# Optimization experiments

Hardware: AMD Instinct MI355X
Metric: run time of the kernel (lower is better)

The kernel has to match this reference:

```python
import jax, jax.numpy as jnp
import numpy as np

B, N, D = 4, 2048, 512

def setup_inputs() -> dict:
    key = jax.random.key(0)
    ks = jax.random.split(key, 7)
    s = 1.0 / np.sqrt(D)
    return {
        "x": jax.random.normal(ks[0], (B, N, D), dtype=jnp.float32),
        "Wq": jax.random.uniform(ks[1], (D, D), jnp.float32, -s, s),
        "bq": jax.random.uniform(ks[2], (D,), jnp.float32, -s, s),
        "Wk": jax.random.uniform(ks[3], (D, D), jnp.float32, -s, s),
        "bk": jax.random.uniform(ks[4], (D,), jnp.float32, -s, s),
        "Wv": jax.random.uniform(ks[5], (D, D), jnp.float32, -s, s),
        "bv": jax.random.uniform(ks[6], (D,), jnp.float32, -s, s),
    }

def reference(x, Wq, bq, Wk, bk, Wv, bv):
    # QKV projections (torch Linear: y = x @ W^T + b)
    q = jnp.einsum('bnd,ed->bne', x, Wq) + bq
    k = jnp.einsum('bnd,ed->bne', x, Wk) + bk
    v = jnp.einsum('bnd,ed->bne', x, Wv) + bv
    scale = 1.0 / jnp.sqrt(jnp.asarray(q.shape[-1], q.dtype))
    scores = jnp.einsum('bqd,bkd->bqk', q, k) * scale  # [B,N,N]
    weights = jax.nn.softmax(scores, axis=-1)
    return jnp.einsum('bqk,bkd->bqd', weights, v)
```

## Files before the change

kernel.cpp:

```cpp
#include <hip/hip_runtime.h>
#include <cstdint>
#include <cstddef>

#define SEQ 2048
#define DIM 512

using floatx4 = __attribute__((ext_vector_type(4))) float;
using halfx8  = __attribute__((ext_vector_type(8))) _Float16;

__device__ __forceinline__ ushort f2h(float f) {
    _Float16 h = (_Float16)f;
    return __builtin_bit_cast(unsigned short, h);
}

__global__ void prep_k(const float* __restrict__ x,
                       const float* __restrict__ Wq, const float* __restrict__ Wk,
                       const float* __restrict__ Wv,
                       const float* __restrict__ bq, const float* __restrict__ bk,
                       const float* __restrict__ bv,
                       ushort* __restrict__ xh, ushort* __restrict__ wcat,
                       float* __restrict__ bcat, float* __restrict__ rowsum) {
    int i = blockIdx.x * 256 + threadIdx.x;
    if (i < 1048576) {
        float4 v = ((const float4*)x)[i];
        ((ushort4*)xh)[i] = make_ushort4(f2h(v.x), f2h(v.y), f2h(v.z), f2h(v.w));
    } else if (i < 1048576 + 196608) {
        int j = i - 1048576;
        int which = j >> 16;
        const float* w = (which == 0) ? Wq : (which == 1) ? Wk : Wv;
        float4 v = ((const float4*)w)[j & 0xFFFF];
        ((ushort4*)wcat)[j] = make_ushort4(f2h(v.x), f2h(v.y), f2h(v.z), f2h(v.w));
    } else if (i < 1048576 + 196608 + 384) {
        int j = i - 1245184;
        const float* bsrc = (j < 128) ? bq : (j < 256) ? bk : bv;
        ((float4*)bcat)[j] = ((const float4*)bsrc)[j & 127];
    } else if (i < 1048576 + 196608 + 384 + 2048) {
        int j = i - 1245568;
        ((float4*)rowsum)[j] = (float4){0.f, 0.f, 0.f, 0.f};
    }
}


template<int EPI>
__global__ __launch_bounds__(512, 4)
void gemm_k(const ushort* __restrict__ A, const ushort* __restrict__ B,
            void* __restrict__ Cout, const float* __restrict__ bias,
            float* __restrict__ rowsum, ushort* __restrict__ vt,
            int lda, int ldb, int ldc, int kIters, float alpha,
            long sA, long sB, long sC)
{
    __shared__ __align__(16) ushort As[2][8192];
    __shared__ __align__(16) ushort Bs[2][4096];
    ushort* Ps = &As[0][0];

    const int tid = threadIdx.x;
    const int bz = blockIdx.z;
    int b, kofs;
    if (EPI == 2) { b = bz & 3; kofs = (bz >> 2) * 512; }
    else          { b = bz; kofs = 0; }
    const ushort* Ab = A + (size_t)b * sA + kofs;
    const ushort* Bb = B + (size_t)b * sB + kofs;

    const int m0 = blockIdx.y * 256;
    const int n0 = blockIdx.x * 128;
    const int lane = tid & 63, wave = tid >> 6;
    const int wm = (wave >> 1) * 64, wn = (wave & 1) * 64;
    const int quad = lane >> 4, l16 = lane & 15;
    const int swz = (l16 >> 1) & 3;

    const int sA0 = tid, sA1 = tid + 512, sBs = tid;
    const int rA0 = sA0 >> 2, rA1 = sA1 >> 2, rB = sBs >> 2;
    const int kA0 = (sA0 & 3) ^ ((rA0 >> 1) & 3);
    const int kA1 = (sA1 & 3) ^ ((rA1 >> 1) & 3);
    const int kB  = (sBs & 3) ^ ((rB  >> 1) & 3);
    const ushort* gA0 = Ab + (size_t)(m0 + rA0) * lda + kA0 * 8;
    const ushort* gA1 = Ab + (size_t)(m0 + rA1) * lda + kA1 * 8;
    const ushort* gB0 = Bb + (size_t)(n0 + rB) * ldb + kB * 8;

#define STAGE(kk, bufi) do {                                                              \
    int ko = (kk) * 32;                                                                   \
    __builtin_amdgcn_global_load_lds((const __attribute__((address_space(1))) uint32_t*)(gA0 + ko), \
        (__attribute__((address_space(3))) uint32_t*)(&As[bufi][sA0 * 8]), 16, 0, 0);     \
    __builtin_amdgcn_global_load_lds((const __attribute__((address_space(1))) uint32_t*)(gA1 + ko), \
        (__attribute__((address_space(3))) uint32_t*)(&As[bufi][sA1 * 8]), 16, 0, 0);     \
    __builtin_amdgcn_global_load_lds((const __attribute__((address_space(1))) uint32_t*)(gB0 + ko), \
        (__attribute__((address_space(3))) uint32_t*)(&Bs[bufi][sBs * 8]), 16, 0, 0);     \
} while (0)

    int ofsA[4], ofsB[4];
#pragma unroll
    for (int mi = 0; mi < 4; mi++)
        ofsA[mi] = ((wm + mi * 16 + l16) * 4 + (quad ^ swz)) * 8;
#pragma unroll
    for (int ni = 0; ni < 4; ni++)
        ofsB[ni] = ((wn + ni * 16 + l16) * 4 + (quad ^ swz)) * 8;

    floatx4 acc[4][4];
#pragma unroll
    for (int i = 0; i < 4; i++)
#pragma unroll
        for (int j = 0; j < 4; j++)
            acc[i][j] = (floatx4){0.f, 0.f, 0.f, 0.f};

    STAGE(0, 0);
    for (int it = 0; it < kIters; ++it) {
        __syncthreads();
        const int buf = it & 1;
        if (it + 1 < kIters) STAGE(it + 1, buf ^ 1);
        halfx8 af[4], bfr[4];
#pragma unroll
        for (int mi = 0; mi < 4; mi++) af[mi] = *(const halfx8*)&As[buf][ofsA[mi]];
#pragma unroll
        for (int ni = 0; ni < 4; ni++) bfr[ni] = *(const halfx8*)&Bs[buf][ofsB[ni]];
#pragma unroll
        for (int mi = 0; mi < 4; mi++)
#pragma unroll
            for (int ni = 0; ni < 4; ni++)
                acc[mi][ni] = __builtin_amdgcn_mfma_f32_16x16x32_f16(af[mi], bfr[ni], acc[mi][ni], 0, 0, 0);
    }
#undef STAGE

    if (EPI == 0 && n0 >= 1024) {
#pragma unroll
        for (int ni = 0; ni < 4; ni++) {
            int col = n0 + wn + ni * 16 + l16;
            float bv = bias[col];
            int e = col - 1024;
#pragma unroll
            for (int mi = 0; mi < 4; mi++) {
                int row0 = m0 + wm + mi * 16 + quad * 4;
                int bb = row0 >> 11;
                int j = row0 & 2047;
                ushort4 pk = make_ushort4(f2h(acc[mi][ni][0] + bv), f2h(acc[mi][ni][1] + bv),
                                          f2h(acc[mi][ni][2] + bv), f2h(acc[mi][ni][3] + bv));
                *(ushort4*)&vt[((size_t)(bb << 9) + e) * 2048 + j] = pk;
            }
        }
    } else {
        float bvv[4];
        if (EPI == 0) {
#pragma unroll
            for (int ni = 0; ni < 4; ni++) bvv[ni] = bias[n0 + wn + ni * 16 + l16];
        }
        float inv[4][4];
        if (EPI == 2) {
#pragma unroll
            for (int mi = 0; mi < 4; mi++)
#pragma unroll
                for (int r = 0; r < 4; r++)
                    inv[mi][r] = __builtin_amdgcn_rcpf(
                        rowsum[b * SEQ + m0 + wm + mi * 16 + quad * 4 + r]);
        }
        size_t base = (EPI == 1) ? (size_t)b * sC : (EPI == 2) ? (size_t)bz * sC : 0;
        __syncthreads();
#pragma unroll
        for (int p = 0; p < 2; ++p) {
            if ((wm >> 7) == p) {
                int wml = wm & 127;
#pragma unroll
                for (int mi = 0; mi < 4; mi++)
#pragma unroll
                    for (int ni = 0; ni < 4; ni++) {
                        int col_l = wn + ni * 16 + l16;
                        int c = col_l >> 3, w = col_l & 7;
#pragma unroll
                        for (int r = 0; r < 4; r++) {
                            int row_l = wml + mi * 16 + quad * 4 + r;
                            float v = (EPI == 1) ? __expf(acc[mi][ni][r] * alpha)
                                    : (EPI == 2) ? acc[mi][ni][r] * inv[mi][r]
                                                 : acc[mi][ni][r] + bvv[ni];
                            Ps[row_l * 128 + ((c ^ (row_l & 7)) << 3) + w] = f2h(v);
                        }
                    }
            }
            __syncthreads();
            int rr = tid >> 2, t3 = tid & 3;
            float s = 0.f;
            ushort* dstrow = (ushort*)Cout + base + (size_t)(m0 + p * 128 + rr) * ldc + n0;
#pragma unroll
            for (int j = 0; j < 4; j++) {
                int c = j * 4 + t3;
                halfx8 pv = *(const halfx8*)&Ps[rr * 128 + ((c ^ (rr & 7)) << 3)];
                if (EPI == 1) {
#pragma unroll
                    for (int e = 0; e < 8; e++) s += (float)pv[e];
                }
                *(halfx8*)(dstrow + c * 8) = pv;
            }
            if (EPI == 1) {
                s += __shfl_xor(s, 1);
                s += __shfl_xor(s, 2);
                if (t3 == 0) atomicAdd(&rowsum[b * SEQ + m0 + p * 128 + rr], s);
            }
            __syncthreads();
        }
    }
}

__global__ void reduce_k(const ushort* __restrict__ part, float* __restrict__ out) {
    int t = blockIdx.x * 256 + threadIdx.x;
    size_t E = (size_t)t * 8;
    int b = (int)(E >> 20);
    size_t le = E & ((1u << 20) - 1);
    float acc[8] = {0,0,0,0,0,0,0,0};
#pragma unroll
    for (int kc = 0; kc < 4; kc++) {
        halfx8 p = *(const halfx8*)&part[(((size_t)(kc * 4 + b)) << 20) + le];
#pragma unroll
        for (int e = 0; e < 8; e++) acc[e] += (float)p[e];
    }
    float4 o0 = {acc[0], acc[1], acc[2], acc[3]};
    float4 o1 = {acc[4], acc[5], acc[6], acc[7]};
    ((float4*)(out + E))[0] = o0;
    ((float4*)(out + E))[1] = o1;
}

extern "C" void kernel_launch(void* const* d_in, const int* in_sizes, int n_in,
                              void* d_out, int out_size, void* d_ws, size_t ws_size,
                              hipStream_t stream) {
    const float* x  = (const float*)d_in[0];
    const float* Wq = (const float*)d_in[1];
    const float* bq = (const float*)d_in[2];
    const float* Wk = (const float*)d_in[3];
    const float* bk = (const float*)d_in[4];
    const float* Wv = (const float*)d_in[5];
    const float* bv = (const float*)d_in[6];
    float* out = (float*)d_out;
    char* ws = (char*)d_ws;

    ushort* partial = (ushort*)(ws);
    ushort* xh      = (ushort*)(ws);
    ushort* wcat    = (ushort*)(ws + 8388608);
    float*  bcat    = (float*)(ws + 9961472);
    float*  rowsum  = (float*)(ws + 33554432);
    ushort* Pb      = (ushort*)(ws + 33587200);
    ushort* vt      = (ushort*)(ws + 67141632);
    ushort* qkh     = (ushort*)(ws + 75530240);

    prep_k<<<4874, 256, 0, stream>>>(x, Wq, Wk, Wv, bq, bk, bv, xh, wcat, bcat, rowsum);

    gemm_k<0><<<dim3(12, 32, 1), 512, 0, stream>>>(
        xh, wcat, qkh, bcat, nullptr, vt, 512, 512, 1024, 16, 1.0f, 0, 0, 0);

    const float scale = 0.04419417382415922f;
    gemm_k<1><<<dim3(16, 8, 4), 512, 0, stream>>>(
        qkh, qkh + 512, Pb, nullptr, rowsum, nullptr, 1024, 1024, 2048, 16, scale,
        (long)SEQ * 1024, (long)SEQ * 1024, (long)SEQ * SEQ);

    gemm_k<2><<<dim3(4, 8, 16), 512, 0, stream>>>(
        Pb, vt, partial, nullptr, rowsum, nullptr, 2048, 2048, 512, 16, 1.0f,
        (long)SEQ * SEQ, (long)DIM * SEQ, (long)SEQ * DIM);

    reduce_k<<<2048, 256, 0, stream>>>(partial, out);
}
```

Baseline: 178.2 us.

## Replace LDS-staged block GEMM with single-wave register-direct 64x64 tiles

Rewrites the shared GEMM kernel so each 64-thread block (one wave) computes a 64x64 tile. Operands are loaded directly from global memory into registers with two-stage register double buffering, replacing the 256x128 block tiles that staged through LDS with global_load_lds and barriers. The epilogue now stages through a small padded LDS tile with no block-wide synchronization, and grids grow accordingly. This removes barrier and LDS-staging overhead but loses cross-wave operand reuse, so global/L2 traffic per FLOP rises substantially.

```diff
diff --git a/kernel.cpp b/kernel.cpp
--- a/kernel.cpp
+++ b/kernel.cpp
@@ -42,16 +42,14 @@
 
 
 template<int EPI>
-__global__ __launch_bounds__(512, 4)
-void gemm_k(const ushort* __restrict__ A, const ushort* __restrict__ B,
+__global__ __launch_bounds__(64, 3)
+void gemm_w(const ushort* __restrict__ A, const ushort* __restrict__ B,
             void* __restrict__ Cout, const float* __restrict__ bias,
             float* __restrict__ rowsum, ushort* __restrict__ vt,
             int lda, int ldb, int ldc, int kIters, float alpha,
             long sA, long sB, long sC)
 {
-    __shared__ __align__(16) ushort As[2][8192];
-    __shared__ __align__(16) ushort Bs[2][4096];
-    ushort* Ps = &As[0][0];
+    __shared__ ushort Ps[64 * 66];
 
     const int tid = threadIdx.x;
     const int bz = blockIdx.z;
@@ -61,39 +59,17 @@
     const ushort* Ab = A + (size_t)b * sA + kofs;
     const ushort* Bb = B + (size_t)b * sB + kofs;
 
-    const int m0 = blockIdx.y * 256;
-    const int n0 = blockIdx.x * 128;
-    const int lane = tid & 63, wave = tid >> 6;
-    const int wm = (wave >> 1) * 64, wn = (wave & 1) * 64;
-    const int quad = lane >> 4, l16 = lane & 15;
-    const int swz = (l16 >> 1) & 3;
-
-    const int sA0 = tid, sA1 = tid + 512, sBs = tid;
-    const int rA0 = sA0 >> 2, rA1 = sA1 >> 2, rB = sBs >> 2;
-    const int kA0 = (sA0 & 3) ^ ((rA0 >> 1) & 3);
-    const int kA1 = (sA1 & 3) ^ ((rA1 >> 1) & 3);
-    const int kB  = (sBs & 3) ^ ((rB  >> 1) & 3);
-    const ushort* gA0 = Ab + (size_t)(m0 + rA0) * lda + kA0 * 8;
-    const ushort* gA1 = Ab + (size_t)(m0 + rA1) * lda + kA1 * 8;
-    const ushort* gB0 = Bb + (size_t)(n0 + rB) * ldb + kB * 8;
-
-#define STAGE(kk, bufi) do {                                                              \
-    int ko = (kk) * 32;                                                                   \
-    __builtin_amdgcn_global_load_lds((const __attribute__((address_space(1))) uint32_t*)(gA0 + ko), \
-        (__attribute__((address_space(3))) uint32_t*)(&As[bufi][sA0 * 8]), 16, 0, 0);     \
-    __builtin_amdgcn_global_load_lds((const __attribute__((address_space(1))) uint32_t*)(gA1 + ko), \
-        (__attribute__((address_space(3))) uint32_t*)(&As[bufi][sA1 * 8]), 16, 0, 0);     \
-    __builtin_amdgcn_global_load_lds((const __attribute__((address_space(1))) uint32_t*)(gB0 + ko), \
-        (__attribute__((address_space(3))) uint32_t*)(&Bs[bufi][sBs * 8]), 16, 0, 0);     \
-} while (0)
-
-    int ofsA[4], ofsB[4];
-#pragma unroll
-    for (int mi = 0; mi < 4; mi++)
-        ofsA[mi] = ((wm + mi * 16 + l16) * 4 + (quad ^ swz)) * 8;
-#pragma unroll
-    for (int ni = 0; ni < 4; ni++)
-        ofsB[ni] = ((wn + ni * 16 + l16) * 4 + (quad ^ swz)) * 8;
+    const int m0 = blockIdx.y * 64;
+    const int n0 = blockIdx.x * 64;
+    const int quad = tid >> 4, l16 = tid & 15;
+
+    const ushort* aP[4];
+    const ushort* bP[4];
+#pragma unroll
+    for (int i = 0; i < 4; i++) {
+        aP[i] = Ab + (size_t)(m0 + i * 16 + l16) * lda + quad * 8;
+        bP[i] = Bb + (size_t)(n0 + i * 16 + l16) * ldb + quad * 8;
+    }
 
     floatx4 acc[4][4];
 #pragma unroll
@@ -102,33 +78,49 @@
         for (int j = 0; j < 4; j++)
             acc[i][j] = (floatx4){0.f, 0.f, 0.f, 0.f};
 
-    STAGE(0, 0);
-    for (int it = 0; it < kIters; ++it) {
-        __syncthreads();
-        const int buf = it & 1;
-        if (it + 1 < kIters) STAGE(it + 1, buf ^ 1);
-        halfx8 af[4], bfr[4];
-#pragma unroll
-        for (int mi = 0; mi < 4; mi++) af[mi] = *(const halfx8*)&As[buf][ofsA[mi]];
-#pragma unroll
-        for (int ni = 0; ni < 4; ni++) bfr[ni] = *(const halfx8*)&Bs[buf][ofsB[ni]];
+    halfx8 a0[4], b0[4], a1[4], b1[4];
+#pragma unroll
+    for (int i = 0; i < 4; i++) {
+        a0[i] = *(const halfx8*)(aP[i]);
+        b0[i] = *(const halfx8*)(bP[i]);
+    }
+
+    for (int it = 0; it < kIters; it += 2) {
+        const int k1 = (it + 1) * 32;
+#pragma unroll
+        for (int i = 0; i < 4; i++) {
+            a1[i] = *(const halfx8*)(aP[i] + k1);
+            b1[i] = *(const halfx8*)(bP[i] + k1);
+        }
 #pragma unroll
         for (int mi = 0; mi < 4; mi++)
 #pragma unroll
             for (int ni = 0; ni < 4; ni++)
-                acc[mi][ni] = __builtin_amdgcn_mfma_f32_16x16x32_f16(af[mi], bfr[ni], acc[mi][ni], 0, 0, 0);
-    }
-#undef STAGE
+                acc[mi][ni] = __builtin_amdgcn_mfma_f32_16x16x32_f16(a0[mi], b0[ni], acc[mi][ni], 0, 0, 0);
+        if (it + 2 < kIters) {
+            const int k2 = (it + 2) * 32;
+#pragma unroll
+            for (int i = 0; i < 4; i++) {
+                a0[i] = *(const halfx8*)(aP[i] + k2);
+                b0[i] = *(const halfx8*)(bP[i] + k2);
+            }
+        }
+#pragma unroll
+        for (int mi = 0; mi < 4; mi++)
+#pragma unroll
+            for (int ni = 0; ni < 4; ni++)
+                acc[mi][ni] = __builtin_amdgcn_mfma_f32_16x16x32_f16(a1[mi], b1[ni], acc[mi][ni], 0, 0, 0);
+    }
 
     if (EPI == 0 && n0 >= 1024) {
 #pragma unroll
         for (int ni = 0; ni < 4; ni++) {
-            int col = n0 + wn + ni * 16 + l16;
+            int col = n0 + ni * 16 + l16;
             float bv = bias[col];
             int e = col - 1024;
 #pragma unroll
             for (int mi = 0; mi < 4; mi++) {
-                int row0 = m0 + wm + mi * 16 + quad * 4;
+                int row0 = m0 + mi * 16 + quad * 4;
                 int bb = row0 >> 11;
                 int j = row0 & 2047;
                 ushort4 pk = make_ushort4(f2h(acc[mi][ni][0] + bv), f2h(acc[mi][ni][1] + bv),
@@ -140,7 +132,7 @@
         float bvv[4];
         if (EPI == 0) {
 #pragma unroll
-            for (int ni = 0; ni < 4; ni++) bvv[ni] = bias[n0 + wn + ni * 16 + l16];
+            for (int ni = 0; ni < 4; ni++) bvv[ni] = bias[n0 + ni * 16 + l16];
         }
         float inv[4][4];
         if (EPI == 2) {
@@ -149,51 +141,39 @@
 #pragma unroll
                 for (int r = 0; r < 4; r++)
                     inv[mi][r] = __builtin_amdgcn_rcpf(
-                        rowsum[b * SEQ + m0 + wm + mi * 16 + quad * 4 + r]);
-        }
+                        rowsum[b * SEQ + m0 + mi * 16 + quad * 4 + r]);
+        }
+#pragma unroll
+        for (int mi = 0; mi < 4; mi++)
+#pragma unroll
+            for (int ni = 0; ni < 4; ni++) {
+                int col_l = ni * 16 + l16;
+#pragma unroll
+                for (int r = 0; r < 4; r++) {
+                    int row_l = mi * 16 + quad * 4 + r;
+                    float v = (EPI == 1) ? __expf(acc[mi][ni][r] * alpha)
+                            : (EPI == 2) ? acc[mi][ni][r] * inv[mi][r]
+                                         : acc[mi][ni][r] + bvv[ni];
+                    Ps[row_l * 66 + col_l] = f2h(v);
+                }
+            }
+        int rr = tid;
         size_t base = (EPI == 1) ? (size_t)b * sC : (EPI == 2) ? (size_t)bz * sC : 0;
-        __syncthreads();
-#pragma unroll
-        for (int p = 0; p < 2; ++p) {
-            if ((wm >> 7) == p) {
-                int wml = wm & 127;
-#pragma unroll
-                for (int mi = 0; mi < 4; mi++)
-#pragma unroll
-                    for (int ni = 0; ni < 4; ni++) {
-                        int col_l = wn + ni * 16 + l16;
-                        int c = col_l >> 3, w = col_l & 7;
-#pragma unroll
-                        for (int r = 0; r < 4; r++) {
-                            int row_l = wml + mi * 16 + quad * 4 + r;
-                            float v = (EPI == 1) ? __expf(acc[mi][ni][r] * alpha)
-                                    : (EPI == 2) ? acc[mi][ni][r] * inv[mi][r]
-                                                 : acc[mi][ni][r] + bvv[ni];
-                            Ps[row_l * 128 + ((c ^ (row_l & 7)) << 3) + w] = f2h(v);
-                        }
-                    }
-            }
-            __syncthreads();
-            int rr = tid >> 2, t3 = tid & 3;
-            float s = 0.f;
-            ushort* dstrow = (ushort*)Cout + base + (size_t)(m0 + p * 128 + rr) * ldc + n0;
-#pragma unroll
-            for (int j = 0; j < 4; j++) {
-                int c = j * 4 + t3;
-                halfx8 pv = *(const halfx8*)&Ps[rr * 128 + ((c ^ (rr & 7)) << 3)];
-                if (EPI == 1) {
-#pragma unroll
-                    for (int e = 0; e < 8; e++) s += (float)pv[e];
-                }
-                *(halfx8*)(dstrow + c * 8) = pv;
-            }
+        ushort* dstrow = (ushort*)Cout + base + (size_t)(m0 + rr) * ldc + n0;
+        float s = 0.f;
+#pragma unroll
+        for (int c = 0; c < 8; c++) {
+            union { uint32_t u[4]; halfx8 h; } U;
+#pragma unroll
+            for (int q = 0; q < 4; q++)
+                U.u[q] = *(const uint32_t*)&Ps[rr * 66 + c * 8 + q * 2];
             if (EPI == 1) {
-                s += __shfl_xor(s, 1);
-                s += __shfl_xor(s, 2);
-                if (t3 == 0) atomicAdd(&rowsum[b * SEQ + m0 + p * 128 + rr], s);
-            }
-            __syncthreads();
-        }
+#pragma unroll
+                for (int e = 0; e < 8; e++) s += (float)U.h[e];
+            }
+            *(halfx8*)(dstrow + c * 8) = U.h;
+        }
+        if (EPI == 1) atomicAdd(&rowsum[b * SEQ + m0 + rr], s);
     }
 }
 
@@ -239,15 +219,15 @@
 
     prep_k<<<4874, 256, 0, stream>>>(x, Wq, Wk, Wv, bq, bk, bv, xh, wcat, bcat, rowsum);
 
-    gemm_k<0><<<dim3(12, 32, 1), 512, 0, stream>>>(
+    gemm_w<0><<<dim3(24, 128, 1), 64, 0, stream>>>(
         xh, wcat, qkh, bcat, nullptr, vt, 512, 512, 1024, 16, 1.0f, 0, 0, 0);
 
     const float scale = 0.04419417382415922f;
-    gemm_k<1><<<dim3(16, 8, 4), 512, 0, stream>>>(
+    gemm_w<1><<<dim3(32, 32, 4), 64, 0, stream>>>(
         qkh, qkh + 512, Pb, nullptr, rowsum, nullptr, 1024, 1024, 2048, 16, scale,
         (long)SEQ * 1024, (long)SEQ * 1024, (long)SEQ * SEQ);
 
-    gemm_k<2><<<dim3(4, 8, 16), 512, 0, stream>>>(
+    gemm_w<2><<<dim3(8, 32, 16), 64, 0, stream>>>(
         Pb, vt, partial, nullptr, rowsum, nullptr, 2048, 2048, 512, 16, 1.0f,
         (long)SEQ * SEQ, (long)DIM * SEQ, (long)SEQ * DIM);
 
```

Measured after the change: 293.8 us. 64.9% more time.

## Template GEMM on M-tile size; use 128-row tiles for QKV and PV GEMMs

Applied to the files above, without the earlier changes.

The GEMM kernel is templated on the M tile height, so the QKV projection and the P@V GEMM can run with 128x128 tiles and 256 threads, while QK^T keeps 256x128. The P@V split-K is reduced from four chunks to two, each twice as long, which halves the partial buffers written and read by the reduce kernel. This trades larger per-block K loops for more blocks in M, aiming at better occupancy and less partial-sum traffic. The risk is lower data reuse per tile and longer serial K loops.

```diff
diff --git a/kernel.cpp b/kernel.cpp
--- a/kernel.cpp
+++ b/kernel.cpp
@@ -12,6 +12,10 @@
     _Float16 h = (_Float16)f;
     return __builtin_bit_cast(unsigned short, h);
 }
+
+#define GLL(g, l) __builtin_amdgcn_global_load_lds( \
+    (const __attribute__((address_space(1))) uint32_t*)(g), \
+    (__attribute__((address_space(3))) uint32_t*)(l), 16, 0, 0)
 
 __global__ void prep_k(const float* __restrict__ x,
                        const float* __restrict__ Wq, const float* __restrict__ Wk,
@@ -41,51 +45,60 @@
 }
 
 
-template<int EPI>
-__global__ __launch_bounds__(512, 4)
+template<int EPI, int TM>
+__global__ __launch_bounds__(TM * 2, 4)
 void gemm_k(const ushort* __restrict__ A, const ushort* __restrict__ B,
             void* __restrict__ Cout, const float* __restrict__ bias,
             float* __restrict__ rowsum, ushort* __restrict__ vt,
             int lda, int ldb, int ldc, int kIters, float alpha,
             long sA, long sB, long sC)
 {
-    __shared__ __align__(16) ushort As[2][8192];
-    __shared__ __align__(16) ushort Bs[2][4096];
-    ushort* Ps = &As[0][0];
+    constexpr int T = TM * 2;
+    __shared__ __align__(16) ushort smem[TM * 64 + 128 * 64];
+    ushort* Ps = smem;
 
     const int tid = threadIdx.x;
     const int bz = blockIdx.z;
     int b, kofs;
-    if (EPI == 2) { b = bz & 3; kofs = (bz >> 2) * 512; }
+    if (EPI == 2) { b = bz & 3; kofs = (bz >> 2) * 1024; }
     else          { b = bz; kofs = 0; }
     const ushort* Ab = A + (size_t)b * sA + kofs;
     const ushort* Bb = B + (size_t)b * sB + kofs;
 
-    const int m0 = blockIdx.y * 256;
+    const int m0 = blockIdx.y * TM;
     const int n0 = blockIdx.x * 128;
     const int lane = tid & 63, wave = tid >> 6;
     const int wm = (wave >> 1) * 64, wn = (wave & 1) * 64;
     const int quad = lane >> 4, l16 = lane & 15;
     const int swz = (l16 >> 1) & 3;
 
-    const int sA0 = tid, sA1 = tid + 512, sBs = tid;
-    const int rA0 = sA0 >> 2, rA1 = sA1 >> 2, rB = sBs >> 2;
+    const int sA0 = tid, sA1 = tid + T;
+    const int rA0 = sA0 >> 2, rA1 = sA1 >> 2;
     const int kA0 = (sA0 & 3) ^ ((rA0 >> 1) & 3);
     const int kA1 = (sA1 & 3) ^ ((rA1 >> 1) & 3);
-    const int kB  = (sBs & 3) ^ ((rB  >> 1) & 3);
     const ushort* gA0 = Ab + (size_t)(m0 + rA0) * lda + kA0 * 8;
     const ushort* gA1 = Ab + (size_t)(m0 + rA1) * lda + kA1 * 8;
-    const ushort* gB0 = Bb + (size_t)(n0 + rB) * ldb + kB * 8;
-
-#define STAGE(kk, bufi) do {                                                              \
-    int ko = (kk) * 32;                                                                   \
-    __builtin_amdgcn_global_load_lds((const __attribute__((address_space(1))) uint32_t*)(gA0 + ko), \
-        (__attribute__((address_space(3))) uint32_t*)(&As[bufi][sA0 * 8]), 16, 0, 0);     \
-    __builtin_amdgcn_global_load_lds((const __attribute__((address_space(1))) uint32_t*)(gA1 + ko), \
-        (__attribute__((address_space(3))) uint32_t*)(&As[bufi][sA1 * 8]), 16, 0, 0);     \
-    __builtin_amdgcn_global_load_lds((const __attribute__((address_space(1))) uint32_t*)(gB0 + ko), \
-        (__attribute__((address_space(3))) uint32_t*)(&Bs[bufi][sBs * 8]), 16, 0, 0);     \
-} while (0)
+    const int rB0 = tid >> 2;
+    const int kB0 = (tid & 3) ^ ((rB0 >> 1) & 3);
+    const ushort* gB0 = Bb + (size_t)(n0 + rB0) * ldb + kB0 * 8;
+    const ushort* gB1 = nullptr;
+    int sB1 = 0;
+    if constexpr (TM == 128) {
+        sB1 = tid + 256;
+        int rB1 = sB1 >> 2;
+        int kB1 = (sB1 & 3) ^ ((rB1 >> 1) & 3);
+        gB1 = Bb + (size_t)(n0 + rB1) * ldb + kB1 * 8;
+    }
+
+    auto STAGE = [&](int kk, int bufi) {
+        int ko = kk * 32;
+        ushort* Ad = smem + bufi * (TM * 32);
+        ushort* Bd = smem + TM * 64 + bufi * 4096;
+        GLL(gA0 + ko, Ad + sA0 * 8);
+        GLL(gA1 + ko, Ad + sA1 * 8);
+        GLL(gB0 + ko, Bd + tid * 8);
+        if constexpr (TM == 128) GLL(gB1 + ko, Bd + sB1 * 8);
+    };
 
     int ofsA[4], ofsB[4];
 #pragma unroll
@@ -107,18 +120,19 @@
         __syncthreads();
         const int buf = it & 1;
         if (it + 1 < kIters) STAGE(it + 1, buf ^ 1);
+        const ushort* Ad = smem + buf * (TM * 32);
+        const ushort* Bd = smem + TM * 64 + buf * 4096;
         halfx8 af[4], bfr[4];
 #pragma unroll
-        for (int mi = 0; mi < 4; mi++) af[mi] = *(const halfx8*)&As[buf][ofsA[mi]];
-#pragma unroll
-        for (int ni = 0; ni < 4; ni++) bfr[ni] = *(const halfx8*)&Bs[buf][ofsB[ni]];
+        for (int mi = 0; mi < 4; mi++) af[mi] = *(const halfx8*)&Ad[ofsA[mi]];
+#pragma unroll
+        for (int ni = 0; ni < 4; ni++) bfr[ni] = *(const halfx8*)&Bd[ofsB[ni]];
 #pragma unroll
         for (int mi = 0; mi < 4; mi++)
 #pragma unroll
             for (int ni = 0; ni < 4; ni++)
                 acc[mi][ni] = __builtin_amdgcn_mfma_f32_16x16x32_f16(af[mi], bfr[ni], acc[mi][ni], 0, 0, 0);
     }
-#undef STAGE
 
     if (EPI == 0 && n0 >= 1024) {
 #pragma unroll
@@ -152,10 +166,11 @@
                         rowsum[b * SEQ + m0 + wm + mi * 16 + quad * 4 + r]);
         }
         size_t base = (EPI == 1) ? (size_t)b * sC : (EPI == 2) ? (size_t)bz * sC : 0;
+        constexpr int NPASS = TM / 128;
         __syncthreads();
 #pragma unroll
-        for (int p = 0; p < 2; ++p) {
-            if ((wm >> 7) == p) {
+        for (int p = 0; p < NPASS; ++p) {
+            if (NPASS == 1 || (wm >> 7) == p) {
                 int wml = wm & 127;
 #pragma unroll
                 for (int mi = 0; mi < 4; mi++)
@@ -174,25 +189,42 @@
                     }
             }
             __syncthreads();
-            int rr = tid >> 2, t3 = tid & 3;
-            float s = 0.f;
-            ushort* dstrow = (ushort*)Cout + base + (size_t)(m0 + p * 128 + rr) * ldc + n0;
-#pragma unroll
-            for (int j = 0; j < 4; j++) {
-                int c = j * 4 + t3;
-                halfx8 pv = *(const halfx8*)&Ps[rr * 128 + ((c ^ (rr & 7)) << 3)];
+            if constexpr (TM == 128) {
+                int rr = tid >> 1, h = tid & 1;
+                float s = 0.f;
+                ushort* dstrow = (ushort*)Cout + base + (size_t)(m0 + rr) * ldc + n0;
+#pragma unroll
+                for (int j = 0; j < 8; j++) {
+                    int c = h * 8 + j;
+                    halfx8 pv = *(const halfx8*)&Ps[rr * 128 + ((c ^ (rr & 7)) << 3)];
+                    if (EPI == 1) {
+#pragma unroll
+                        for (int e = 0; e < 8; e++) s += (float)pv[e];
+                    }
+                    *(halfx8*)(dstrow + c * 8) = pv;
+                }
+                if (EPI == 1) atomicAdd(&rowsum[b * SEQ + m0 + rr], s);
+            } else {
+                int rr = tid >> 2, t3 = tid & 3;
+                float s = 0.f;
+                ushort* dstrow = (ushort*)Cout + base + (size_t)(m0 + p * 128 + rr) * ldc + n0;
+#pragma unroll
+                for (int j = 0; j < 4; j++) {
+                    int c = j * 4 + t3;
+                    halfx8 pv = *(const halfx8*)&Ps[rr * 128 + ((c ^ (rr & 7)) << 3)];
+                    if (EPI == 1) {
+#pragma unroll
+                        for (int e = 0; e < 8; e++) s += (float)pv[e];
+                    }
+                    *(halfx8*)(dstrow + c * 8) = pv;
+                }
                 if (EPI == 1) {
-#pragma unroll
-                    for (int e = 0; e < 8; e++) s += (float)pv[e];
+                    s += __shfl_xor(s, 1);
+                    s += __shfl_xor(s, 2);
+                    if (t3 == 0) atomicAdd(&rowsum[b * SEQ + m0 + p * 128 + rr], s);
                 }
-                *(halfx8*)(dstrow + c * 8) = pv;
             }
-            if (EPI == 1) {
-                s += __shfl_xor(s, 1);
-                s += __shfl_xor(s, 2);
-                if (t3 == 0) atomicAdd(&rowsum[b * SEQ + m0 + p * 128 + rr], s);
-            }
-            __syncthreads();
+            if (p + 1 < NPASS) __syncthreads();
         }
     }
 }
@@ -204,7 +236,7 @@
     size_t le = E & ((1u << 20) - 1);
     float acc[8] = {0,0,0,0,0,0,0,0};
 #pragma unroll
-    for (int kc = 0; kc < 4; kc++) {
+    for (int kc = 0; kc < 2; kc++) {
         halfx8 p = *(const halfx8*)&part[(((size_t)(kc * 4 + b)) << 20) + le];
 #pragma unroll
         for (int e = 0; e < 8; e++) acc[e] += (float)p[e];
@@ -239,16 +271,16 @@
 
     prep_k<<<4874, 256, 0, stream>>>(x, Wq, Wk, Wv, bq, bk, bv, xh, wcat, bcat, rowsum);
 
-    gemm_k<0><<<dim3(12, 32, 1), 512, 0, stream>>>(
+    gemm_k<0, 128><<<dim3(12, 64, 1), 256, 0, stream>>>(
         xh, wcat, qkh, bcat, nullptr, vt, 512, 512, 1024, 16, 1.0f, 0, 0, 0);
 
     const float scale = 0.04419417382415922f;
-    gemm_k<1><<<dim3(16, 8, 4), 512, 0, stream>>>(
+    gemm_k<1, 256><<<dim3(16, 8, 4), 512, 0, stream>>>(
         qkh, qkh + 512, Pb, nullptr, rowsum, nullptr, 1024, 1024, 2048, 16, scale,
         (long)SEQ * 1024, (long)SEQ * 1024, (long)SEQ * SEQ);
 
-    gemm_k<2><<<dim3(4, 8, 16), 512, 0, stream>>>(
-        Pb, vt, partial, nullptr, rowsum, nullptr, 2048, 2048, 512, 16, 1.0f,
+    gemm_k<2, 128><<<dim3(4, 16, 8), 256, 0, stream>>>(
+        Pb, vt, partial, nullptr, rowsum, nullptr, 2048, 2048, 512, 32, 1.0f,
         (long)SEQ * SEQ, (long)DIM * SEQ, (long)SEQ * DIM);
 
     reduce_k<<<2048, 256, 0, stream>>>(partial, out);
```

New measurement: 167.4 us. -6.1%, faster.
